# Kernel tuning notes

Hardware: AMD Instinct MI355X
Metric: run time of the kernel (lower is better)

The kernel has to match this reference:

```python
import jax, jax.numpy as jnp
from jax import lax
import numpy as np

DIM = 64
NUM_HEADS = 1
SR_RATIO = 8
LN_EPS = 1e-3  # Keras LayerNormalization default


def setup_inputs() -> dict:
    key = jax.random.key(0)
    ks = jax.random.split(key, 8)
    B, H, W = 8, 128, 128
    N, C = H * W, DIM
    s = 0.02
    x = jax.random.normal(ks[0], (B, N, C), dtype=jnp.float32)
    Wq = jax.random.normal(ks[1], (C, C), dtype=jnp.float32) * s
    Wkv = jax.random.normal(ks[2], (C, 2 * C), dtype=jnp.float32) * s
    sr_kernel = jax.random.normal(ks[3], (SR_RATIO, SR_RATIO, C, C), dtype=jnp.float32) * s
    sr_bias = jnp.zeros((C,), dtype=jnp.float32)
    ln_gamma = jnp.ones((C,), dtype=jnp.float32)
    ln_beta = jnp.zeros((C,), dtype=jnp.float32)
    Wproj = jax.random.normal(ks[4], (C, C), dtype=jnp.float32) * s
    bproj = jnp.zeros((C,), dtype=jnp.float32)
    return {"x": x, "H": H, "W": W, "Wq": Wq, "Wkv": Wkv,
            "sr_kernel": sr_kernel, "sr_bias": sr_bias,
            "ln_gamma": ln_gamma, "ln_beta": ln_beta,
            "Wproj": Wproj, "bproj": bproj}


def reference(x, H, W, Wq, Wkv, sr_kernel, sr_bias, ln_gamma, ln_beta, Wproj, bproj):
    B, N, C = x.shape
    nh = NUM_HEADS
    hd = C // nh
    scale = hd ** -0.5

    # q: [B, nh, N, hd]
    q = (x @ Wq).reshape(B, N, nh, hd).transpose(0, 2, 1, 3)

    # spatial-reduction KV path (faithful to the TF code, incl. its
    # transpose-then-reshape ordering)
    x_ = jnp.transpose(x, (0, 2, 1)).reshape(B, H, W, C)
    x_ = lax.conv_general_dilated(
        x_, sr_kernel, window_strides=(SR_RATIO, SR_RATIO), padding="VALID",
        dimension_numbers=("NHWC", "HWIO", "NHWC")) + sr_bias
    M = x_.shape[1] * x_.shape[2]
    x_ = x_.reshape(B, M, C)
    # LayerNorm over last axis
    mu = jnp.mean(x_, axis=-1, keepdims=True)
    var = jnp.mean(jnp.square(x_ - mu), axis=-1, keepdims=True)
    x_ = (x_ - mu) * lax.rsqrt(var + LN_EPS) * ln_gamma + ln_beta

    kv = (x_ @ Wkv).reshape(B, M, 2, nh, hd).transpose(2, 0, 3, 1, 4)
    k, v = kv[0], kv[1]  # [B, nh, M, hd]

    attn = jax.nn.softmax(jnp.einsum("bhnd,bhmd->bhnm", q, k) * scale, axis=-1)
    out = jnp.einsum("bhnm,bhmd->bhnd", attn, v)
    out = out.transpose(0, 2, 1, 3).reshape(B, N, C)
    return out @ Wproj + bproj
```

## Files before the change

kernel.cpp:

```cpp
#include <hip/hip_runtime.h>
#include <hip/hip_bf16.h>

#define B_   8
#define N_   16384
#define C_   64
#define M_   256
#define NPB  1048576

typedef __attribute__((ext_vector_type(8))) short short8v;
typedef __attribute__((ext_vector_type(16))) float f32x16;
typedef __attribute__((ext_vector_type(4)))  float f32x4;

union FragU { short8v s8; unsigned u[4]; };

__device__ inline unsigned pkbf(float a, float b) {
  union { __hip_bfloat162 h2; unsigned u; } cv;
  cv.h2 = __float22bfloat162_rn(make_float2(a, b));
  return cv.u;
}
__device__ inline unsigned short bfbits(float a) {
  union { __hip_bfloat16 h; unsigned short u; } cv;
  cv.h = __float2bfloat16(a);
  return cv.u;
}
__device__ inline float bf2f(unsigned short u) {
  union { unsigned u; float f; } cv;
  cv.u = ((unsigned)u) << 16;
  return cv.f;
}
__device__ inline short8v ld8(const unsigned short* p) {
  return *(const short8v*)p;
}

__device__ inline void plswap(unsigned &a, unsigned &b) {
#if __has_builtin(__builtin_amdgcn_permlane32_swap)
  typedef unsigned uint2v __attribute__((ext_vector_type(2)));
  uint2v r = __builtin_amdgcn_permlane32_swap(a, b, false, false);
  a = r[0]; b = r[1];
#else
  asm volatile("v_permlane32_swap_b32 %0, %1" : "+v"(a), "+v"(b));
#endif
}

__device__ inline void repack16(const f32x16 s, FragU& f0, FragU& f1) {
  #pragma unroll
  for (int h = 0; h < 2; ++h) {
    FragU& f = h ? f1 : f0;
    unsigned a0 = pkbf(s[8*h+0], s[8*h+1]);
    unsigned a1 = pkbf(s[8*h+2], s[8*h+3]);
    unsigned a2 = pkbf(s[8*h+4], s[8*h+5]);
    unsigned a3 = pkbf(s[8*h+6], s[8*h+7]);
    plswap(a0, a2);
    plswap(a1, a3);
    f.u[0] = a0; f.u[1] = a1; f.u[2] = a2; f.u[3] = a3;
  }
}

__global__ __launch_bounds__(256) void prep(const float* __restrict__ Wq,
                                            const float* __restrict__ Wp,
                                            const float* __restrict__ Kw,
                                            unsigned short* __restrict__ wql,
                                            unsigned short* __restrict__ wpl,
                                            unsigned short* __restrict__ kbt) {
  const int i = blockIdx.x * 256 + threadIdx.x;
  if (i < 8192) {
    const int idx = i & 4095, sel = i >> 12;
    const int j = idx & 7, l = (idx >> 3) & 63, tt = (idx >> 9) & 3, ct = idx >> 11;
    const int ci = 16 * tt + 8 * (l >> 5) + j, co = (l & 31) + 32 * ct;
    const float* W = sel ? Wp : Wq;
    (sel ? wpl : wql)[idx] = bfbits(W[ci * 64 + co]);
  } else if (i < 8192 + 262144) {
    const int idx = i - 8192;
    const int j = idx & 7, l = (idx >> 3) & 63, s = (idx >> 9) & 15;
    const int w = (idx >> 13) & 3, kw = idx >> 15;
    const int e = s * 32 + 8 * (l >> 4) + j;
    const int par = e >> 8, ci = (e >> 2) & 63, jj = e & 3;
    const int kh = 2 * jj + par, co = 16 * w + (l & 15);
    kbt[idx] = bfbits(Kw[(size_t)((kh * 8 + kw) * 64 + ci) * 64 + co]);
  }
}

__global__ __launch_bounds__(256) void conv_mfma(const float* __restrict__ x,
                                                 const unsigned short* __restrict__ kbt,
                                                 unsigned short* __restrict__ xrb) {
  const int kw = blockIdx.x & 7;
  const int ow = (blockIdx.x >> 3) & 15;
  const int b  = blockIdx.x >> 7;
  const int t  = threadIdx.x, w = t >> 6, l = t & 63;
  const int oh = l & 15, kg = l >> 4;

  const float* xb = x + (size_t)b * NPB + (size_t)((ow * 8 + kw) * 64) * 64 + oh * 4;
  const unsigned short* kb = kbt + (size_t)(((kw * 4 + w) * 16) * 64 + l) * 8;

  f32x4 acc = {0.f, 0.f, 0.f, 0.f};
  #pragma unroll
  for (int s = 0; s < 16; ++s) {
    const int eb  = s * 32 + kg * 8;
    const int par = (s >= 8) ? 1 : 0;
    const int ci  = ((s * 8) + kg * 2) & 63;
    const float* ax = xb + (size_t)par * 524288 + ci * 64;
    const float4 a0 = *(const float4*)(ax);
    const float4 a1 = *(const float4*)(ax + 64);
    (void)eb;
    FragU af;
    af.u[0] = pkbf(a0.x, a0.y); af.u[1] = pkbf(a0.z, a0.w);
    af.u[2] = pkbf(a1.x, a1.y); af.u[3] = pkbf(a1.z, a1.w);
    const short8v bfrag = ld8(kb + s * 512);
    acc = __builtin_amdgcn_mfma_f32_16x16x32_bf16(af.s8, bfrag, acc, 0, 0, 0);
  }
  unsigned short* dst = xrb + (size_t)kw * 131072
                      + ((size_t)b * 256 + ow) * 64 + w * 16 + (l & 15);
  #pragma unroll
  for (int r = 0; r < 4; ++r)
    dst[(size_t)((l >> 4) * 4 + r) * 1024] = bfbits(acc[r]);
}

__global__ __launch_bounds__(256) void ln_kv(const unsigned short* __restrict__ xrb,
                                             const float* __restrict__ sr_bias,
                                             const float* __restrict__ gamma,
                                             const float* __restrict__ beta,
                                             const float* __restrict__ Wkv,
                                             unsigned short* __restrict__ kbl,
                                             unsigned short* __restrict__ vbl) {
  const int w   = threadIdx.x >> 6;
  const int row = blockIdx.x * 4 + w;
  const int c   = threadIdx.x & 63;
  float val = sr_bias[c];
  #pragma unroll
  for (int s = 0; s < 8; ++s)
    val += bf2f(xrb[(size_t)s * 131072 + (size_t)row * 64 + c]);

  float sum = val;
  #pragma unroll
  for (int off = 32; off; off >>= 1) sum += __shfl_xor(sum, off, 64);
  const float mu = sum * (1.f / 64.f);
  const float d  = val - mu;
  float vs = d * d;
  #pragma unroll
  for (int off = 32; off; off >>= 1) vs += __shfl_xor(vs, off, 64);
  const float rs = rsqrtf(vs * (1.f / 64.f) + 1e-3f);
  const float ln = d * rs * gamma[c] + beta[c];

  __shared__ float lnrow[4][64];
  lnrow[w][c] = ln;
  __syncthreads();

  float ka = 0.f, va = 0.f;
  #pragma unroll 8
  for (int cc = 0; cc < 64; ++cc) {
    const float l = lnrow[w][cc];
    ka += l * Wkv[cc * 128 + c];
    va += l * Wkv[cc * 128 + 64 + c];
  }
  const int m = row & 255, bb = row >> 8;
  kbl[(size_t)bb * 16384
      + (size_t)((((m >> 5) * 4 + (c >> 4)) * 64) + (m & 31) + 32 * ((c >> 3) & 1)) * 8
      + (c & 7)] = bfbits(ka);
  vbl[(size_t)bb * 16384
      + (size_t)(((c >> 5) * 8 + (m >> 5)) * 2 + ((m >> 4) & 1)) * 512
      + (size_t)((c & 31) + 32 * ((m >> 3) & 1)) * 8
      + (m & 7)] = bfbits(va);
}

__global__ __launch_bounds__(256, 4) void attn_mfma(const float* __restrict__ x,
                                                    const unsigned short* __restrict__ kbl,
                                                    const unsigned short* __restrict__ vbl,
                                                    const unsigned short* __restrict__ wql,
                                                    const unsigned short* __restrict__ wpl,
                                                    const float* __restrict__ bp,
                                                    float* __restrict__ out) {
  __shared__ float ot[128 * 68];
  const int t    = threadIdx.x;
  const int w    = t >> 6;
  const int l    = t & 63;
  const int l31  = l & 31;
  const int hi   = l >> 5;
  const int b    = blockIdx.x >> 7;
  const int tile = blockIdx.x & 127;
  const size_t nrow = (size_t)b * N_ + (size_t)tile * 128;
  const int qrow = w * 32 + l31;

  const float* xrow = x + (nrow + qrow) * 64;
  FragU xb[4];
  #pragma unroll
  for (int tt = 0; tt < 4; ++tt) {
    const float* p = xrow + 16 * tt + 8 * hi;
    const float4 x0 = *(const float4*)(p);
    const float4 x1 = *(const float4*)(p + 4);
    xb[tt].u[0] = pkbf(x0.x, x0.y); xb[tt].u[1] = pkbf(x0.z, x0.w);
    xb[tt].u[2] = pkbf(x1.x, x1.y); xb[tt].u[3] = pkbf(x1.z, x1.w);
  }

  FragU Qb[4];
  #pragma unroll
  for (int ct = 0; ct < 2; ++ct) {
    f32x16 qa;
    #pragma unroll
    for (int r = 0; r < 16; ++r) qa[r] = 0.f;
    #pragma unroll
    for (int tt = 0; tt < 4; ++tt) {
      const short8v aw = ld8(wql + (size_t)((ct * 4 + tt) * 64 + l) * 8);
      qa = __builtin_amdgcn_mfma_f32_32x32x16_bf16(aw, xb[tt].s8, qa, 0, 0, 0);
    }
    repack16(qa, Qb[2 * ct], Qb[2 * ct + 1]);
  }

  const unsigned short* kfp = kbl + (size_t)b * 16384 + l * 8;
  const unsigned short* vfp = vbl + (size_t)b * 16384 + l * 8;
  f32x16 O0, O1;
  #pragma unroll
  for (int r = 0; r < 16; ++r) { O0[r] = 0.f; O1[r] = 0.f; }
  float ss = 0.f;

  #pragma unroll
  for (int kt = 0; kt < 8; ++kt) {
    const short8v vf00 = ld8(vfp + (size_t)((kt * 2 + 0) * 512));
    const short8v vf01 = ld8(vfp + (size_t)((kt * 2 + 1) * 512));
    const short8v vf10 = ld8(vfp + (size_t)(((8 + kt) * 2 + 0) * 512));
    const short8v vf11 = ld8(vfp + (size_t)(((8 + kt) * 2 + 1) * 512));
    f32x16 S;
    #pragma unroll
    for (int r = 0; r < 16; ++r) S[r] = 0.f;
    #pragma unroll
    for (int tt = 0; tt < 4; ++tt) {
      const short8v ak = ld8(kfp + (size_t)((kt * 4 + tt) * 512));
      S = __builtin_amdgcn_mfma_f32_32x32x16_bf16(ak, Qb[tt].s8, S, 0, 0, 0);
    }
    f32x16 P;
    #pragma unroll
    for (int r = 0; r < 16; ++r) {
      const float pv = __expf(S[r] * 0.125f);
      P[r] = pv; ss += pv;
    }
    FragU f0, f1;
    repack16(P, f0, f1);
    O0 = __builtin_amdgcn_mfma_f32_32x32x16_bf16(vf00, f0.s8, O0, 0, 0, 0);
    O0 = __builtin_amdgcn_mfma_f32_32x32x16_bf16(vf01, f1.s8, O0, 0, 0, 0);
    O1 = __builtin_amdgcn_mfma_f32_32x32x16_bf16(vf10, f0.s8, O1, 0, 0, 0);
    O1 = __builtin_amdgcn_mfma_f32_32x32x16_bf16(vf11, f1.s8, O1, 0, 0, 0);
  }

  ss += __shfl_xor(ss, 32);
  const float inv = 1.f / ss;
  #pragma unroll
  for (int r = 0; r < 16; ++r) { O0[r] *= inv; O1[r] *= inv; }
  FragU Ob[4];
  repack16(O0, Ob[0], Ob[1]);
  repack16(O1, Ob[2], Ob[3]);

  #pragma unroll
  for (int ct = 0; ct < 2; ++ct) {
    f32x16 F;
    #pragma unroll
    for (int r = 0; r < 16; ++r) F[r] = 0.f;
    #pragma unroll
    for (int tt = 0; tt < 4; ++tt) {
      const short8v aw = ld8(wpl + (size_t)((ct * 4 + tt) * 64 + l) * 8);
      F = __builtin_amdgcn_mfma_f32_32x32x16_bf16(aw, Ob[tt].s8, F, 0, 0, 0);
    }
    #pragma unroll
    for (int g = 0; g < 4; ++g) {
      const int co = 32 * ct + 8 * g + 4 * hi;
      const float4 bb = *(const float4*)(bp + co);
      *(float4*)&ot[qrow * 68 + co] =
          make_float4(F[4 * g + 0] + bb.x, F[4 * g + 1] + bb.y,
                      F[4 * g + 2] + bb.z, F[4 * g + 3] + bb.w);
    }
  }

  __syncthreads();
  float4* out4 = (float4*)(out + nrow * 64);
  #pragma unroll
  for (int i = 0; i < 8; ++i) {
    const int idx = i * 256 + t;
    const int row = idx >> 4, c4 = idx & 15;
    out4[idx] = *(const float4*)&ot[row * 68 + c4 * 4];
  }
}

extern "C" void kernel_launch(void* const* d_in, const int* in_sizes, int n_in,
                              void* d_out, int out_size, void* d_ws, size_t ws_size,
                              hipStream_t stream) {
  const float* x   = (const float*)d_in[0];
  const float* Wq  = (const float*)d_in[3];
  const float* Wkv = (const float*)d_in[4];
  const float* Kw  = (const float*)d_in[5];
  const float* sb  = (const float*)d_in[6];
  const float* gam = (const float*)d_in[7];
  const float* bet = (const float*)d_in[8];
  const float* Wp  = (const float*)d_in[9];
  const float* bp  = (const float*)d_in[10];
  float* out = (float*)d_out;

  unsigned short* xrb = (unsigned short*)d_ws;
  unsigned short* kbl = xrb + 1048576;
  unsigned short* vbl = kbl + 131072;
  unsigned short* wql = vbl + 131072;
  unsigned short* wpl = wql + 4096;
  unsigned short* kbt = wpl + 4096;

  prep<<<1057, 256, 0, stream>>>(Wq, Wp, Kw, wql, wpl, kbt);
  conv_mfma<<<1024, 256, 0, stream>>>(x, kbt, xrb);
  ln_kv<<<512, 256, 0, stream>>>(xrb, sb, gam, bet, Wkv, kbl, vbl);
  attn_mfma<<<1024, 256, 0, stream>>>(x, kbl, vbl, wql, wpl, bp, out);
}
```

Baseline: 50.77 us.

## Fold Wq into K and Wproj into V to drop per-tile projections

Uses associativity so the key path absorbs Wq and the softmax scale (K' = LN·Wk·Wqᵀ/8), and the value path absorbs Wproj (V' = LN·Wv·Wproj). The attention kernel then multiplies raw bf16 x directly against K' and writes normalized O plus bias, with no Q projection or output projection MFMAs and no repacks. The folded weights are computed once in the prep kernel on the small 256-row KV side. Rounding changes because x goes to bf16 before the fused product and the folded weights are rounded differently.

New measurement: 46.85 us. -7.7%, faster.

```diff
diff --git a/kernel.cpp b/kernel.cpp
--- a/kernel.cpp
+++ b/kernel.cpp
@@ -59,24 +59,32 @@
 __global__ __launch_bounds__(256) void prep(const float* __restrict__ Wq,
                                             const float* __restrict__ Wp,
                                             const float* __restrict__ Kw,
-                                            unsigned short* __restrict__ wql,
-                                            unsigned short* __restrict__ wpl,
-                                            unsigned short* __restrict__ kbt) {
-  const int i = blockIdx.x * 256 + threadIdx.x;
-  if (i < 8192) {
-    const int idx = i & 4095, sel = i >> 12;
-    const int j = idx & 7, l = (idx >> 3) & 63, tt = (idx >> 9) & 3, ct = idx >> 11;
-    const int ci = 16 * tt + 8 * (l >> 5) + j, co = (l & 31) + 32 * ct;
-    const float* W = sel ? Wp : Wq;
-    (sel ? wpl : wql)[idx] = bfbits(W[ci * 64 + co]);
-  } else if (i < 8192 + 262144) {
-    const int idx = i - 8192;
+                                            const float* __restrict__ Wkv,
+                                            unsigned short* __restrict__ kbt,
+                                            float* __restrict__ wkp,
+                                            float* __restrict__ wvp) {
+  const int gi = blockIdx.x;
+  if (gi < 1024) {
+    const int idx = gi * 256 + threadIdx.x;
     const int j = idx & 7, l = (idx >> 3) & 63, s = (idx >> 9) & 15;
     const int w = (idx >> 13) & 3, kw = idx >> 15;
     const int e = s * 32 + 8 * (l >> 4) + j;
     const int par = e >> 8, ci = (e >> 2) & 63, jj = e & 3;
     const int kh = 2 * jj + par, co = 16 * w + (l & 15);
     kbt[idx] = bfbits(Kw[(size_t)((kh * 8 + kw) * 64 + ci) * 64 + co]);
+  } else {
+    const int idx = (gi - 1024) * 256 + threadIdx.x;
+    const int c = idx & 63, cc = (idx >> 6) & 63, sel = idx >> 12;
+    float s = 0.f;
+    if (sel == 0) {
+      #pragma unroll 8
+      for (int d = 0; d < 64; ++d) s += Wkv[cc * 128 + d] * Wq[c * 64 + d];
+      wkp[cc * 64 + c] = s * 0.125f;
+    } else {
+      #pragma unroll 8
+      for (int d = 0; d < 64; ++d) s += Wkv[cc * 128 + 64 + d] * Wp[d * 64 + c];
+      wvp[cc * 64 + c] = s;
+    }
   }
 }
 
@@ -95,13 +103,11 @@
   f32x4 acc = {0.f, 0.f, 0.f, 0.f};
   #pragma unroll
   for (int s = 0; s < 16; ++s) {
-    const int eb  = s * 32 + kg * 8;
     const int par = (s >= 8) ? 1 : 0;
     const int ci  = ((s * 8) + kg * 2) & 63;
     const float* ax = xb + (size_t)par * 524288 + ci * 64;
     const float4 a0 = *(const float4*)(ax);
     const float4 a1 = *(const float4*)(ax + 64);
-    (void)eb;
     FragU af;
     af.u[0] = pkbf(a0.x, a0.y); af.u[1] = pkbf(a0.z, a0.w);
     af.u[2] = pkbf(a1.x, a1.y); af.u[3] = pkbf(a1.z, a1.w);
@@ -119,7 +125,8 @@
                                              const float* __restrict__ sr_bias,
                                              const float* __restrict__ gamma,
                                              const float* __restrict__ beta,
-                                             const float* __restrict__ Wkv,
+                                             const float* __restrict__ wkp,
+                                             const float* __restrict__ wvp,
                                              unsigned short* __restrict__ kbl,
                                              unsigned short* __restrict__ vbl) {
   const int w   = threadIdx.x >> 6;
@@ -149,8 +156,8 @@
   #pragma unroll 8
   for (int cc = 0; cc < 64; ++cc) {
     const float l = lnrow[w][cc];
-    ka += l * Wkv[cc * 128 + c];
-    va += l * Wkv[cc * 128 + 64 + c];
+    ka += l * wkp[cc * 64 + c];
+    va += l * wvp[cc * 64 + c];
   }
   const int m = row & 255, bb = row >> 8;
   kbl[(size_t)bb * 16384
@@ -165,8 +172,6 @@
 __global__ __launch_bounds__(256, 4) void attn_mfma(const float* __restrict__ x,
                                                     const unsigned short* __restrict__ kbl,
                                                     const unsigned short* __restrict__ vbl,
-                                                    const unsigned short* __restrict__ wql,
-                                                    const unsigned short* __restrict__ wpl,
                                                     const float* __restrict__ bp,
                                                     float* __restrict__ out) {
   __shared__ float ot[128 * 68];
@@ -191,20 +196,6 @@
     xb[tt].u[2] = pkbf(x1.x, x1.y); xb[tt].u[3] = pkbf(x1.z, x1.w);
   }
 
-  FragU Qb[4];
-  #pragma unroll
-  for (int ct = 0; ct < 2; ++ct) {
-    f32x16 qa;
-    #pragma unroll
-    for (int r = 0; r < 16; ++r) qa[r] = 0.f;
-    #pragma unroll
-    for (int tt = 0; tt < 4; ++tt) {
-      const short8v aw = ld8(wql + (size_t)((ct * 4 + tt) * 64 + l) * 8);
-      qa = __builtin_amdgcn_mfma_f32_32x32x16_bf16(aw, xb[tt].s8, qa, 0, 0, 0);
-    }
-    repack16(qa, Qb[2 * ct], Qb[2 * ct + 1]);
-  }
-
   const unsigned short* kfp = kbl + (size_t)b * 16384 + l * 8;
   const unsigned short* vfp = vbl + (size_t)b * 16384 + l * 8;
   f32x16 O0, O1;
@@ -224,12 +215,12 @@
     #pragma unroll
     for (int tt = 0; tt < 4; ++tt) {
       const short8v ak = ld8(kfp + (size_t)((kt * 4 + tt) * 512));
-      S = __builtin_amdgcn_mfma_f32_32x32x16_bf16(ak, Qb[tt].s8, S, 0, 0, 0);
+      S = __builtin_amdgcn_mfma_f32_32x32x16_bf16(ak, xb[tt].s8, S, 0, 0, 0);
     }
     f32x16 P;
     #pragma unroll
     for (int r = 0; r < 16; ++r) {
-      const float pv = __expf(S[r] * 0.125f);
+      const float pv = __expf(S[r]);
       P[r] = pv; ss += pv;
     }
     FragU f0, f1;
@@ -243,28 +234,20 @@
   ss += __shfl_xor(ss, 32);
   const float inv = 1.f / ss;
   #pragma unroll
-  for (int r = 0; r < 16; ++r) { O0[r] *= inv; O1[r] *= inv; }
-  FragU Ob[4];
-  repack16(O0, Ob[0], Ob[1]);
-  repack16(O1, Ob[2], Ob[3]);
-
-  #pragma unroll
-  for (int ct = 0; ct < 2; ++ct) {
-    f32x16 F;
-    #pragma unroll
-    for (int r = 0; r < 16; ++r) F[r] = 0.f;
-    #pragma unroll
-    for (int tt = 0; tt < 4; ++tt) {
-      const short8v aw = ld8(wpl + (size_t)((ct * 4 + tt) * 64 + l) * 8);
-      F = __builtin_amdgcn_mfma_f32_32x32x16_bf16(aw, Ob[tt].s8, F, 0, 0, 0);
-    }
-    #pragma unroll
-    for (int g = 0; g < 4; ++g) {
-      const int co = 32 * ct + 8 * g + 4 * hi;
+  for (int g = 0; g < 4; ++g) {
+    {
+      const int co = 8 * g + 4 * hi;
       const float4 bb = *(const float4*)(bp + co);
       *(float4*)&ot[qrow * 68 + co] =
-          make_float4(F[4 * g + 0] + bb.x, F[4 * g + 1] + bb.y,
-                      F[4 * g + 2] + bb.z, F[4 * g + 3] + bb.w);
+          make_float4(O0[4 * g + 0] * inv + bb.x, O0[4 * g + 1] * inv + bb.y,
+                      O0[4 * g + 2] * inv + bb.z, O0[4 * g + 3] * inv + bb.w);
+    }
+    {
+      const int co = 32 + 8 * g + 4 * hi;
+      const float4 bb = *(const float4*)(bp + co);
+      *(float4*)&ot[qrow * 68 + co] =
+          make_float4(O1[4 * g + 0] * inv + bb.x, O1[4 * g + 1] * inv + bb.y,
+                      O1[4 * g + 2] * inv + bb.z, O1[4 * g + 3] * inv + bb.w);
     }
   }
 
@@ -295,12 +278,12 @@
   unsigned short* xrb = (unsigned short*)d_ws;
   unsigned short* kbl = xrb + 1048576;
   unsigned short* vbl = kbl + 131072;
-  unsigned short* wql = vbl + 131072;
-  unsigned short* wpl = wql + 4096;
-  unsigned short* kbt = wpl + 4096;
-
-  prep<<<1057, 256, 0, stream>>>(Wq, Wp, Kw, wql, wpl, kbt);
+  unsigned short* kbt = vbl + 131072;
+  float* wkp = (float*)(kbt + 262144);
+  float* wvp = wkp + 4096;
+
+  prep<<<1056, 256, 0, stream>>>(Wq, Wp, Kw, Wkv, kbt, wkp, wvp);
   conv_mfma<<<1024, 256, 0, stream>>>(x, kbt, xrb);
-  ln_kv<<<512, 256, 0, stream>>>(xrb, sb, gam, bet, Wkv, kbl, vbl);
-  attn_mfma<<<1024, 256, 0, stream>>>(x, kbl, vbl, wql, wpl, bp, out);
-}
+  ln_kv<<<512, 256, 0, stream>>>(xrb, sb, gam, bet, wkp, wvp, kbl, vbl);
+  attn_mfma<<<1024, 256, 0, stream>>>(x, kbl, vbl, bp, out);
+}
```
